# Optimization experiments

Hardware: AMD Instinct MI355X
Metric: run time of the kernel (lower is better)

The kernel has to match this reference:

```python
import jax, jax.numpy as jnp
import numpy as np

B, SL, H = 8, 512, 768
NS, W = 256, 32            # num_spans, max_span_width (static pad width)
NH = 12
HD = H // NH
FFN_I = int(H * 4)         # int(output_dim * ffn_ratio)
LN_EPS = 1e-5
NEG = -1e9


def _pos_encoding(seq_len, hidden):
    pos = jnp.arange(seq_len, dtype=jnp.float32)[:, None]
    div = jnp.exp(jnp.arange(0, hidden, 2, dtype=jnp.float32) * (-np.log(10000.0) / hidden))
    pe = jnp.zeros((seq_len, hidden), jnp.float32)
    pe = pe.at[:, 0::2].set(jnp.sin(pos * div))
    pe = pe.at[:, 1::2].set(jnp.cos(pos * div))
    return pe


def _layernorm(x, g, b):
    mu = jnp.mean(x, axis=-1, keepdims=True)
    var = jnp.mean(jnp.square(x - mu), axis=-1, keepdims=True)
    return (x - mu) * jax.lax.rsqrt(var + LN_EPS) * g + b


def setup_inputs() -> dict:
    key = jax.random.key(0)
    ks = jax.random.split(key, 16)
    token_reps = jax.random.normal(ks[0], (B, SL, H), jnp.float32)
    starts = jax.random.randint(ks[1], (B, NS), 0, SL - W)
    widths = jax.random.randint(ks[2], (B, NS), 0, W + 1)  # includes empty spans
    span_ids = jnp.stack([starts, starts + widths], axis=-1).astype(jnp.int64)
    s = 0.02
    return {
        "token_reps": token_reps,
        "span_ids": span_ids,
        "dummy_query": jax.random.normal(ks[3], (1, 1, H), jnp.float32),
        "in_proj_w": jax.random.normal(ks[4], (3 * H, H), jnp.float32) * s,
        "in_proj_b": jnp.zeros((3 * H,), jnp.float32),
        "out_proj_w": jax.random.normal(ks[5], (H, H), jnp.float32) * s,
        "out_proj_b": jnp.zeros((H,), jnp.float32),
        "ln_g": jnp.ones((H,), jnp.float32),
        "ln_b": jnp.zeros((H,), jnp.float32),
        "ffn_w1": jax.random.normal(ks[6], (FFN_I, H), jnp.float32) * s,
        "ffn_b1": jnp.zeros((FFN_I,), jnp.float32),
        "ffn_w2": jax.random.normal(ks[7], (H, FFN_I), jnp.float32) * s,
        "ffn_b2": jnp.zeros((H,), jnp.float32),
        "pooling": 1,
    }


def reference(token_reps, span_ids, dummy_query, in_proj_w, in_proj_b,
              out_proj_w, out_proj_b, ln_g, ln_b,
              ffn_w1, ffn_b1, ffn_w2, ffn_b2, pooling):
    # sequence positional encoding (dropout=0 / eval mode)
    pe = _pos_encoding(SL, H)
    tok = token_reps + pe[None, :, :]

    starts = span_ids[..., 0]                        # (B, NS)
    lengths = span_ids[..., 1] - span_ids[..., 0]    # (B, NS)
    offs = jnp.arange(W)
    pos = starts[..., None] + offs                   # (B, NS, W)
    valid = offs[None, None, :] < lengths[..., None] # (B, NS, W) bool
    idx = jnp.clip(pos, 0, SL - 1)
    # vectorized span gather -> padded tensor (B, NS, W, H), zeros on padding
    spans = tok[jnp.arange(B)[:, None, None], idx]
    spans = spans * valid[..., None].astype(tok.dtype)

    N = B * NS
    spans = spans.reshape(N, W, H)
    valid_f = valid.reshape(N, W)

    Wq, Wk, Wv = jnp.split(in_proj_w, 3, axis=0)
    bq, bk, bv = jnp.split(in_proj_b, 3, axis=0)

    q0 = dummy_query[0, 0]                            # (H,)
    q = (q0 @ Wq.T + bq).reshape(NH, HD)              # (NH, HD)
    k = (spans @ Wk.T + bk).reshape(N, W, NH, HD)
    v = (spans @ Wv.T + bv).reshape(N, W, NH, HD)

    scores = jnp.einsum('hd,nwhd->nhw', q, k) / np.sqrt(HD)
    scores = jnp.where(valid_f[:, None, :], scores, NEG)
    attn = jax.nn.softmax(scores, axis=-1)            # (N, NH, W)
    ctx = jnp.einsum('nhw,nwhd->nhd', attn, v).reshape(N, H)
    attn_out = ctx @ out_proj_w.T + out_proj_b        # (N, H)

    x = _layernorm(attn_out + q0, ln_g, ln_b)
    h = jnp.maximum(x @ ffn_w1.T + ffn_b1, 0.0)
    x = _layernorm((h @ ffn_w2.T + ffn_b2) + x, ln_g, ln_b)

    out = x.reshape(B, NS, H)
    out = jnp.where((lengths > 0)[..., None], out, 0.0)
    return out
```

## Files before the change

### kernel.cpp

```cpp
#include <hip/hip_runtime.h>
#include <hip/hip_bf16.h>
#include <cstdint>

#define Bb 8
#define SLh 512
#define Hh 768
#define NSs 256
#define Ww 32
#define NHh 12
#define HDd 64
#define FFN_I 3072
#define NTOK (Bb*SLh)
#define NSPAN (Bb*NSs)
#define NVS 832

typedef __attribute__((ext_vector_type(8))) __bf16 bf16x8;
typedef __attribute__((ext_vector_type(4))) float f32x4;

__device__ __forceinline__ short f2bf(float f) {
  unsigned u = __builtin_bit_cast(unsigned, f);
  unsigned r = (u + 0x7fffu + ((u >> 16) & 1u)) >> 16;
  return (short)r;
}
__device__ __forceinline__ float bflo(unsigned u) { return __builtin_bit_cast(float, u << 16); }
__device__ __forceinline__ float bfhi(unsigned u) { return __builtin_bit_cast(float, u & 0xffff0000u); }

__device__ __forceinline__ void gload16(const void* g, void* l) {
  __builtin_amdgcn_global_load_lds(
      (__attribute__((address_space(1))) void*)(const_cast<void*>(g)),
      (__attribute__((address_space(3))) void*)l, 16, 0, 0);
}

__global__ __launch_bounds__(192) void tok_kernel(const float* __restrict__ tr,
                                                  short* __restrict__ tok) {
  int row = blockIdx.x;
  int s = row & (SLh - 1);
  int c0 = threadIdx.x * 4;
  float4 v = *(const float4*)(tr + (size_t)row * Hh + c0);
  const float kinv = -9.210340371976184f / (float)Hh;
  float f0 = __expf((float)c0 * kinv);
  float f1 = __expf((float)(c0 + 2) * kinv);
  float s0, cc0, s1, cc1;
  __sincosf((float)s * f0, &s0, &cc0);
  __sincosf((float)s * f1, &s1, &cc1);
  v.x += s0; v.y += cc0; v.z += s1; v.w += cc1;
  short4 o{f2bf(v.x), f2bf(v.y), f2bf(v.z), f2bf(v.w)};
  *(short4*)(tok + (size_t)row * Hh + c0) = o;
}

__global__ __launch_bounds__(256) void cast4(const float* __restrict__ s0,
                                             const float* __restrict__ s1,
                                             const float* __restrict__ s2,
                                             const float* __restrict__ s3,
                                             short* __restrict__ d0,
                                             short* __restrict__ d1,
                                             short* __restrict__ d2,
                                             short* __restrict__ d3) {
  int b = blockIdx.x;
  if (b >= 5760) {
    int i = (b - 5760) * 256 + threadIdx.x;
    ((short4*)d0)[149760 + i] = short4{0, 0, 0, 0};
    return;
  }
  const float* s; short* d; int off;
  if (b < 576)       { s = s0; d = d0; off = b; }
  else if (b < 1152) { s = s1; d = d1; off = b - 576; }
  else if (b < 3456) { s = s2; d = d2; off = b - 1152; }
  else               { s = s3; d = d3; off = b - 3456; }
  int i = off * 256 + threadIdx.x;
  float4 v = ((const float4*)s)[i];
  short4 o{f2bf(v.x), f2bf(v.y), f2bf(v.z), f2bf(v.w)};
  ((short4*)d)[i] = o;
}

__global__ __launch_bounds__(64) void prep_qb(const float* __restrict__ dq,
                                              const float* __restrict__ ipw,
                                              const float* __restrict__ ipb,
                                              const float* __restrict__ opb,
                                              float* __restrict__ qsv,
                                              float* __restrict__ bias2,
                                              float* __restrict__ bvs) {
  int b = blockIdx.x, lane = threadIdx.x;
  if (b == 12) { if (lane < 52) bvs[780 + lane] = 0.f; return; }
  int h = b * 64 + lane;
  const float4* wr = (const float4*)(ipw + (size_t)h * Hh);
  const float4* qv = (const float4*)dq;
  float acc = 0.f;
  for (int j = 0; j < Hh / 4; ++j) {
    float4 w4 = wr[j], q4 = qv[j];
    acc += w4.x * q4.x + w4.y * q4.y + w4.z * q4.z + w4.w * q4.w;
  }
  acc += ipb[h];
  float qs = acc * 0.125f;
  qsv[h] = qs;
  bias2[h] = opb[h] + dq[h];
  bvs[h] = ipb[2 * Hh + h];
  float t = qs * ipb[Hh + h];
#pragma unroll
  for (int o = 32; o; o >>= 1) t += __shfl_xor(t, o);
  if (lane == 0) bvs[768 + b] = t;
}

__global__ __launch_bounds__(64) void qk_kernel(const float* __restrict__ ipw,
                                                const float* __restrict__ qsv,
                                                short* __restrict__ vsw) {
  int h = blockIdx.x, dc = blockIdx.y, lane = threadIdx.x;
  int d = dc * 64 + lane;
  const float* wk = ipw + (size_t)(Hh + h * 64) * Hh + d;
  const float* qh = qsv + h * 64;
  float a = 0.f;
#pragma unroll 8
  for (int e = 0; e < 64; ++e) a += qh[e] * wk[(size_t)e * Hh];
  vsw[(size_t)(768 + h) * Hh + d] = f2bf(a);
}

template <int EPI, int BN>
__global__ __launch_bounds__(256, BN == 64 ? 3 : 2)
void gemm_bt(const short* __restrict__ A,
             const short* __restrict__ Bt,
             const float* __restrict__ bias,
             float* __restrict__ Cf,
             short* __restrict__ Cb,
             int M, int N, int ldk, int Kc,
             int nx, int ypp) {
  constexpr int NI = BN / 32;
  __shared__ __align__(16) char Al[2][128 * 128];
  __shared__ __align__(16) char Bl[2][BN * 128];
  const int tid = threadIdx.x;
  const int lane = tid & 63, wave = tid >> 6;
  const int wm = wave >> 1, wn = wave & 1;
  const int bid = blockIdx.x, xcd = bid & 7, ii = bid >> 3;
  const int iy = ii / nx;
  const int by = xcd * ypp + iy, bx = ii - iy * nx;
  const int row0 = by * 128, col0 = bx * BN;
  const int kbase = blockIdx.y * Kc;
  const int l15 = lane & 15, hi = lane >> 4;
  f32x4 acc[4][NI] = {};
  const int nk = Kc >> 6;
  const int srow = tid >> 3, sslot = tid & 7;

  auto stage = [&](int kt, int bi) {
    const short* Agp = A + (size_t)row0 * ldk + kbase + kt * 64;
    const short* Bgp = Bt + (size_t)col0 * ldk + kbase + kt * 64;
#pragma unroll
    for (int j = 0; j < 4; ++j) {
      int row = j * 32 + srow;
      int col = (sslot ^ (row & 7)) << 3;
      gload16(Agp + (size_t)row * ldk + col,
              &Al[bi][0] + (size_t)(j * 256 + wave * 64) * 16);
    }
#pragma unroll
    for (int j = 0; j < NI; ++j) {
      int row = j * 32 + srow;
      int col = (sslot ^ (row & 7)) << 3;
      gload16(Bgp + (size_t)row * ldk + col,
              &Bl[bi][0] + (size_t)(j * 256 + wave * 64) * 16);
    }
  };

  stage(0, 0);
  for (int kt = 0; kt < nk; ++kt) {
    const int cur = kt & 1;
    if (kt + 1 < nk) {
      stage(kt + 1, cur ^ 1);
      if constexpr (BN == 64)
        asm volatile("s_waitcnt vmcnt(6)" ::: "memory");
      else
        asm volatile("s_waitcnt vmcnt(8)" ::: "memory");
    } else {
      asm volatile("s_waitcnt vmcnt(0)" ::: "memory");
    }
    __builtin_amdgcn_s_barrier();
    asm volatile("" ::: "memory");
    bf16x8 fa[2][4], fb[2][NI];
#pragma unroll
    for (int kk = 0; kk < 2; ++kk) {
#pragma unroll
      for (int i = 0; i < 4; ++i) {
        int Ra = wm * 64 + i * 16 + l15;
        fa[kk][i] = *(const bf16x8*)(&Al[cur][0] + (size_t)Ra * 128 +
                                     (((kk * 4 + hi) ^ (Ra & 7)) << 4));
      }
#pragma unroll
      for (int i = 0; i < NI; ++i) {
        int Rb = wn * (BN / 2) + i * 16 + l15;
        fb[kk][i] = *(const bf16x8*)(&Bl[cur][0] + (size_t)Rb * 128 +
                                     (((kk * 4 + hi) ^ (Rb & 7)) << 4));
      }
    }
#pragma unroll
    for (int kk = 0; kk < 2; ++kk)
#pragma unroll
      for (int mi = 0; mi < 4; ++mi)
#pragma unroll
        for (int ni = 0; ni < NI; ++ni)
          acc[mi][ni] = __builtin_amdgcn_mfma_f32_16x16x32_bf16(fa[kk][mi], fb[kk][ni], acc[mi][ni], 0, 0, 0);
    asm volatile("" ::: "memory");
    __builtin_amdgcn_s_barrier();
  }

  float* dst = (EPI == 3) ? (Cf + (size_t)blockIdx.y * M * N) : Cf;
#pragma unroll
  for (int mi = 0; mi < 4; ++mi) {
#pragma unroll
    for (int ni = 0; ni < NI; ++ni) {
      int colb = col0 + wn * (BN / 2) + ni * 16 + l15;
      float bv = (EPI == 3) ? 0.f : bias[colb];
#pragma unroll
      for (int r = 0; r < 4; ++r) {
        int rowb = row0 + wm * 64 + mi * 16 + hi * 4 + r;
        float v = acc[mi][ni][r] + bv;
        if (EPI == 1) {
          Cb[(size_t)rowb * N + colb] = f2bf(fmaxf(v, 0.f));
        } else if (EPI == 3) {
          dst[(size_t)rowb * N + colb] = v;
        } else {
          if (colb < 768) Cb[(size_t)rowb * 768 + colb] = f2bf(v);
          else if (colb < 780) Cf[(size_t)rowb * 12 + (colb - 768)] = v;
        }
      }
    }
  }
}

__global__ __launch_bounds__(384) void attn_kernel(const short* __restrict__ Vb,
                                                   const float* __restrict__ S,
                                                   const int* __restrict__ sid,
                                                   short* __restrict__ ctx) {
  int bid = blockIdx.x;
  int n = ((bid & 7) << 8) | (bid >> 3);
  int b = n >> 8;
  __shared__ int posV[Ww], tS[Ww];
  __shared__ float attnL[NHh][Ww];
  __shared__ int lenS;
  int tid = threadIdx.x;
  if (tid < Ww) {
    int st = sid[2 * n], en = sid[2 * n + 1];
    int p = st + tid;
    p = p < 0 ? 0 : (p > SLh - 1 ? SLh - 1 : p);
    int t = b * SLh + p;
    posV[tid] = t * Hh;
    tS[tid] = t * 12;
    if (tid == 0) lenS = en - st;
  }
  __syncthreads();
  int len = lenS;
  int h = tid >> 5, w = tid & 31;
  float score = (w < len) ? S[tS[w] + h] : -1e9f;
  float m = score;
#pragma unroll
  for (int o = 16; o; o >>= 1) m = fmaxf(m, __shfl_xor(m, o, 32));
  float e = __expf(score - m);
  float ssum = e;
#pragma unroll
  for (int o = 16; o; o >>= 1) ssum += __shfl_xor(ssum, o, 32);
  attnL[h][w] = e / ssum;
  __syncthreads();
  int hh = tid >> 5, dp = tid & 31;
  float a0 = 0.f, a1 = 0.f;
#pragma unroll
  for (int w2 = 0; w2 < Ww; ++w2) {
    float aw = attnL[hh][w2];
    unsigned u = *(const unsigned*)(Vb + posV[w2] + hh * HDd + 2 * dp);
    a0 += aw * bflo(u);
    a1 += aw * bfhi(u);
  }
  unsigned packed = (unsigned)(unsigned short)f2bf(a0) | ((unsigned)(unsigned short)f2bf(a1) << 16);
  ((unsigned*)ctx)[(size_t)n * (Hh / 2) + tid] = packed;
}

__global__ __launch_bounds__(256) void ln_kernel(const float* __restrict__ Y2,
                                                 const float* __restrict__ bias2,
                                                 const float* __restrict__ g,
                                                 const float* __restrict__ b,
                                                 float* __restrict__ xf,
                                                 short* __restrict__ xb) {
  const size_t SL = (size_t)NSPAN * Hh;
  int row = blockIdx.x;
  int tid = threadIdx.x;
  float v[3]; float s1 = 0.f, s2 = 0.f;
#pragma unroll
  for (int i = 0; i < 3; ++i) {
    int c = tid + 256 * i;
    size_t idx = (size_t)row * Hh + c;
    v[i] = Y2[idx] + Y2[idx + SL] + bias2[c];
    s1 += v[i]; s2 += v[i] * v[i];
  }
  __shared__ float r1[4], r2[4];
#pragma unroll
  for (int o = 32; o; o >>= 1) { s1 += __shfl_xor(s1, o); s2 += __shfl_xor(s2, o); }
  int lane = tid & 63, wv = tid >> 6;
  if (lane == 0) { r1[wv] = s1; r2[wv] = s2; }
  __syncthreads();
  s1 = r1[0] + r1[1] + r1[2] + r1[3];
  s2 = r2[0] + r2[1] + r2[2] + r2[3];
  float mu = s1 * (1.f / Hh);
  float var = s2 * (1.f / Hh) - mu * mu;
  float is = rsqrtf(var + 1e-5f);
#pragma unroll
  for (int i = 0; i < 3; ++i) {
    int c = tid + 256 * i;
    float o = (v[i] - mu) * is * g[c] + b[c];
    xf[(size_t)row * Hh + c] = o;
    xb[(size_t)row * Hh + c] = f2bf(o);
  }
}

__global__ __launch_bounds__(256) void ln_final(const float* __restrict__ Y4,
                                                const float* __restrict__ b2,
                                                const float* __restrict__ xf,
                                                const float* __restrict__ g,
                                                const float* __restrict__ b,
                                                const int* __restrict__ sid,
                                                float* __restrict__ out) {
  const size_t SL = (size_t)NSPAN * Hh;
  int row = blockIdx.x;
  int len = sid[2 * row + 1] - sid[2 * row];
  int tid = threadIdx.x;
  float v[3]; float s1 = 0.f, s2 = 0.f;
#pragma unroll
  for (int i = 0; i < 3; ++i) {
    int c = tid + 256 * i;
    size_t idx = (size_t)row * Hh + c;
    v[i] = Y4[idx] + Y4[idx + SL] + Y4[idx + 2 * SL] + Y4[idx + 3 * SL]
         + b2[c] + xf[idx];
    s1 += v[i]; s2 += v[i] * v[i];
  }
  __shared__ float r1[4], r2[4];
#pragma unroll
  for (int o = 32; o; o >>= 1) { s1 += __shfl_xor(s1, o); s2 += __shfl_xor(s2, o); }
  int lane = tid & 63, wv = tid >> 6;
  if (lane == 0) { r1[wv] = s1; r2[wv] = s2; }
  __syncthreads();
  s1 = r1[0] + r1[1] + r1[2] + r1[3];
  s2 = r2[0] + r2[1] + r2[2] + r2[3];
  float mu = s1 * (1.f / Hh);
  float var = s2 * (1.f / Hh) - mu * mu;
  float is = rsqrtf(var + 1e-5f);
  float keep = (len > 0) ? 1.f : 0.f;
#pragma unroll
  for (int i = 0; i < 3; ++i) {
    int c = tid + 256 * i;
    float o = ((v[i] - mu) * is * g[c] + b[c]) * keep;
    out[(size_t)row * Hh + c] = o;
  }
}

extern "C" void kernel_launch(void* const* d_in, const int* in_sizes, int n_in,
                              void* d_out, int out_size, void* d_ws, size_t ws_size,
                              hipStream_t stream) {
  const float* token_reps = (const float*)d_in[0];
  const int* span_ids = (const int*)d_in[1];
  const float* dq = (const float*)d_in[2];
  const float* ipw = (const float*)d_in[3];
  const float* ipb = (const float*)d_in[4];
  const float* opw = (const float*)d_in[5];
  const float* opb = (const float*)d_in[6];
  const float* lng = (const float*)d_in[7];
  const float* lnb = (const float*)d_in[8];
  const float* w1 = (const float*)d_in[9];
  const float* b1 = (const float*)d_in[10];
  const float* w2 = (const float*)d_in[11];
  const float* b2 = (const float*)d_in[12];
  float* out = (float*)d_out;

  char* p = (char*)d_ws;
  auto alloc = [&](size_t bytes) { void* r = p; p += (bytes + 255) & ~(size_t)255; return r; };
  short* tokb = (short*)alloc((size_t)NTOK * Hh * 2);
  short* vsw  = (short*)alloc((size_t)NVS * Hh * 2);
  short* outw = (short*)alloc((size_t)Hh * Hh * 2);
  short* w1b  = (short*)alloc((size_t)FFN_I * Hh * 2);
  short* w2b  = (short*)alloc((size_t)Hh * FFN_I * 2);
  float* qsv  = (float*)alloc(Hh * 4);
  float* bias2= (float*)alloc(Hh * 4);
  float* bvs  = (float*)alloc(NVS * 4);
  float* S    = (float*)alloc((size_t)NTOK * 12 * 4);
  short* Vb   = (short*)alloc((size_t)NTOK * Hh * 2);
  short* ctxb = (short*)alloc((size_t)NSPAN * Hh * 2);
  float* attnY= (float*)alloc((size_t)2 * NSPAN * Hh * 4);
  float* xf   = (float*)alloc((size_t)NSPAN * Hh * 4);
  short* xb   = (short*)alloc((size_t)NSPAN * Hh * 2);
  short* hb   = (short*)alloc((size_t)NSPAN * FFN_I * 2);
  float* y2   = (float*)alloc((size_t)4 * NSPAN * Hh * 4);

  tok_kernel<<<NTOK, 192, 0, stream>>>(token_reps, tokb);
  cast4<<<5799, 256, 0, stream>>>(ipw + (size_t)2 * Hh * Hh, opw, w1, w2,
                                  vsw, outw, w1b, w2b);
  prep_qb<<<13, 64, 0, stream>>>(dq, ipw, ipb, opb, qsv, bias2, bvs);
  qk_kernel<<<dim3(12, 12), 64, 0, stream>>>(ipw, qsv, vsw);
  gemm_bt<4, 64><<<dim3(416, 1), 256, 0, stream>>>(tokb, vsw, bvs, S, Vb,
                                                   NTOK, NVS, Hh, Hh, 13, 4);
  attn_kernel<<<NSPAN, 384, 0, stream>>>(Vb, S, span_ids, ctxb);
  gemm_bt<3, 64><<<dim3(192, 2), 256, 0, stream>>>(ctxb, outw, nullptr, attnY, nullptr,
                                                   NSPAN, Hh, Hh, Hh / 2, 12, 2);
  ln_kernel<<<NSPAN, 256, 0, stream>>>(attnY, bias2, lng, lnb, xf, xb);
  gemm_bt<1, 128><<<dim3(384, 1), 256, 0, stream>>>(xb, w1b, b1, nullptr, hb,
                                                    NSPAN, FFN_I, Hh, Hh, 24, 2);
  gemm_bt<3, 128><<<dim3(96, 4), 256, 0, stream>>>(hb, w2b, nullptr, y2, nullptr,
                                                   NSPAN, Hh, FFN_I, FFN_I / 4, 6, 2);
  ln_final<<<NSPAN, 256, 0, stream>>>(y2, b2, xf, lng, lnb, span_ids, out);
}
```

Before: 204.2 us.

## Merge prep kernels, add BM template, retile FFN GEMMs and split out-proj K further

```diff
diff --git a/kernel.cpp b/kernel.cpp
--- a/kernel.cpp
+++ b/kernel.cpp
@@ -31,91 +31,88 @@
       (__attribute__((address_space(3))) void*)l, 16, 0, 0);
 }
 
-__global__ __launch_bounds__(192) void tok_kernel(const float* __restrict__ tr,
-                                                  short* __restrict__ tok) {
-  int row = blockIdx.x;
-  int s = row & (SLh - 1);
-  int c0 = threadIdx.x * 4;
-  float4 v = *(const float4*)(tr + (size_t)row * Hh + c0);
-  const float kinv = -9.210340371976184f / (float)Hh;
-  float f0 = __expf((float)c0 * kinv);
-  float f1 = __expf((float)(c0 + 2) * kinv);
-  float s0, cc0, s1, cc1;
-  __sincosf((float)s * f0, &s0, &cc0);
-  __sincosf((float)s * f1, &s1, &cc1);
-  v.x += s0; v.y += cc0; v.z += s1; v.w += cc1;
-  short4 o{f2bf(v.x), f2bf(v.y), f2bf(v.z), f2bf(v.w)};
-  *(short4*)(tok + (size_t)row * Hh + c0) = o;
-}
-
-__global__ __launch_bounds__(256) void cast4(const float* __restrict__ s0,
-                                             const float* __restrict__ s1,
-                                             const float* __restrict__ s2,
-                                             const float* __restrict__ s3,
-                                             short* __restrict__ d0,
-                                             short* __restrict__ d1,
-                                             short* __restrict__ d2,
-                                             short* __restrict__ d3) {
-  int b = blockIdx.x;
-  if (b >= 5760) {
-    int i = (b - 5760) * 256 + threadIdx.x;
-    ((short4*)d0)[149760 + i] = short4{0, 0, 0, 0};
+__global__ __launch_bounds__(256) void prep_all(const float* __restrict__ tr,
+                                                const float* __restrict__ wv,
+                                                const float* __restrict__ wo,
+                                                const float* __restrict__ w1,
+                                                const float* __restrict__ w2,
+                                                short* __restrict__ tok,
+                                                short* __restrict__ vsw,
+                                                short* __restrict__ outw,
+                                                short* __restrict__ w1b,
+                                                short* __restrict__ w2b) {
+  int b = blockIdx.x, tid = threadIdx.x;
+  if (b < 3072) {
+    int i4 = b * 256 + tid;
+    int row = i4 / 192;
+    int c0 = (i4 - row * 192) * 4;
+    int s = row & (SLh - 1);
+    float4 v = ((const float4*)tr)[i4];
+    const float kinv = -9.210340371976184f / (float)Hh;
+    float f0 = __expf((float)c0 * kinv);
+    float f1 = __expf((float)(c0 + 2) * kinv);
+    float s0, cc0, s1, cc1;
+    __sincosf((float)s * f0, &s0, &cc0);
+    __sincosf((float)s * f1, &s1, &cc1);
+    v.x += s0; v.y += cc0; v.z += s1; v.w += cc1;
+    ((short4*)tok)[i4] = short4{f2bf(v.x), f2bf(v.y), f2bf(v.z), f2bf(v.w)};
     return;
   }
+  if (b >= 8832) {
+    int i = (b - 8832) * 256 + tid;
+    ((short4*)vsw)[149760 + i] = short4{0, 0, 0, 0};
+    return;
+  }
   const float* s; short* d; int off;
-  if (b < 576)       { s = s0; d = d0; off = b; }
-  else if (b < 1152) { s = s1; d = d1; off = b - 576; }
-  else if (b < 3456) { s = s2; d = d2; off = b - 1152; }
-  else               { s = s3; d = d3; off = b - 3456; }
-  int i = off * 256 + threadIdx.x;
+  if (b < 3648)      { s = wv; d = vsw;  off = b - 3072; }
+  else if (b < 4224) { s = wo; d = outw; off = b - 3648; }
+  else if (b < 6528) { s = w1; d = w1b;  off = b - 4224; }
+  else               { s = w2; d = w2b;  off = b - 6528; }
+  int i = off * 256 + tid;
   float4 v = ((const float4*)s)[i];
-  short4 o{f2bf(v.x), f2bf(v.y), f2bf(v.z), f2bf(v.w)};
-  ((short4*)d)[i] = o;
-}
-
-__global__ __launch_bounds__(64) void prep_qb(const float* __restrict__ dq,
-                                              const float* __restrict__ ipw,
-                                              const float* __restrict__ ipb,
-                                              const float* __restrict__ opb,
-                                              float* __restrict__ qsv,
-                                              float* __restrict__ bias2,
-                                              float* __restrict__ bvs) {
-  int b = blockIdx.x, lane = threadIdx.x;
-  if (b == 12) { if (lane < 52) bvs[780 + lane] = 0.f; return; }
-  int h = b * 64 + lane;
-  const float4* wr = (const float4*)(ipw + (size_t)h * Hh);
+  ((short4*)d)[i] = short4{f2bf(v.x), f2bf(v.y), f2bf(v.z), f2bf(v.w)};
+}
+
+__global__ __launch_bounds__(64) void qkprep(const float* __restrict__ dq,
+                                             const float* __restrict__ ipw,
+                                             const float* __restrict__ ipb,
+                                             const float* __restrict__ opb,
+                                             float* __restrict__ bias2,
+                                             float* __restrict__ bvs,
+                                             short* __restrict__ vsw) {
+  int h = blockIdx.x, dc = blockIdx.y, lane = threadIdx.x;
+  int hl = h * 64 + lane;
+  const float4* wr = (const float4*)(ipw + (size_t)hl * Hh);
   const float4* qv = (const float4*)dq;
   float acc = 0.f;
   for (int j = 0; j < Hh / 4; ++j) {
     float4 w4 = wr[j], q4 = qv[j];
     acc += w4.x * q4.x + w4.y * q4.y + w4.z * q4.z + w4.w * q4.w;
   }
-  acc += ipb[h];
-  float qs = acc * 0.125f;
-  qsv[h] = qs;
-  bias2[h] = opb[h] + dq[h];
-  bvs[h] = ipb[2 * Hh + h];
-  float t = qs * ipb[Hh + h];
-#pragma unroll
-  for (int o = 32; o; o >>= 1) t += __shfl_xor(t, o);
-  if (lane == 0) bvs[768 + b] = t;
-}
-
-__global__ __launch_bounds__(64) void qk_kernel(const float* __restrict__ ipw,
-                                                const float* __restrict__ qsv,
-                                                short* __restrict__ vsw) {
-  int h = blockIdx.x, dc = blockIdx.y, lane = threadIdx.x;
+  float qs = (acc + ipb[hl]) * 0.125f;
+  if (dc == 12) {
+    bias2[hl] = opb[hl] + dq[hl];
+    bvs[hl] = ipb[2 * Hh + hl];
+    float t = qs * ipb[Hh + hl];
+#pragma unroll
+    for (int o = 32; o; o >>= 1) t += __shfl_xor(t, o);
+    if (lane == 0) bvs[768 + h] = t;
+    if (h == 0 && lane < 52) bvs[780 + lane] = 0.f;
+    return;
+  }
+  __shared__ float qh[64];
+  qh[lane] = qs;
+  __syncthreads();
   int d = dc * 64 + lane;
   const float* wk = ipw + (size_t)(Hh + h * 64) * Hh + d;
-  const float* qh = qsv + h * 64;
   float a = 0.f;
 #pragma unroll 8
   for (int e = 0; e < 64; ++e) a += qh[e] * wk[(size_t)e * Hh];
   vsw[(size_t)(768 + h) * Hh + d] = f2bf(a);
 }
 
-template <int EPI, int BN>
-__global__ __launch_bounds__(256, BN == 64 ? 3 : 2)
+template <int EPI, int BM, int BN>
+__global__ __launch_bounds__(256, 3)
 void gemm_bt(const short* __restrict__ A,
              const short* __restrict__ Bt,
              const float* __restrict__ bias,
@@ -123,8 +120,8 @@
              short* __restrict__ Cb,
              int M, int N, int ldk, int Kc,
              int nx, int ypp) {
-  constexpr int NI = BN / 32;
-  __shared__ __align__(16) char Al[2][128 * 128];
+  constexpr int MI = BM / 32, NI = BN / 32;
+  __shared__ __align__(16) char Al[2][BM * 128];
   __shared__ __align__(16) char Bl[2][BN * 128];
   const int tid = threadIdx.x;
   const int lane = tid & 63, wave = tid >> 6;
@@ -132,10 +129,10 @@
   const int bid = blockIdx.x, xcd = bid & 7, ii = bid >> 3;
   const int iy = ii / nx;
   const int by = xcd * ypp + iy, bx = ii - iy * nx;
-  const int row0 = by * 128, col0 = bx * BN;
+  const int row0 = by * BM, col0 = bx * BN;
   const int kbase = blockIdx.y * Kc;
   const int l15 = lane & 15, hi = lane >> 4;
-  f32x4 acc[4][NI] = {};
+  f32x4 acc[MI][NI] = {};
   const int nk = Kc >> 6;
   const int srow = tid >> 3, sslot = tid & 7;
 
@@ -143,7 +140,7 @@
     const short* Agp = A + (size_t)row0 * ldk + kbase + kt * 64;
     const short* Bgp = Bt + (size_t)col0 * ldk + kbase + kt * 64;
 #pragma unroll
-    for (int j = 0; j < 4; ++j) {
+    for (int j = 0; j < MI; ++j) {
       int row = j * 32 + srow;
       int col = (sslot ^ (row & 7)) << 3;
       gload16(Agp + (size_t)row * ldk + col,
@@ -163,21 +160,18 @@
     const int cur = kt & 1;
     if (kt + 1 < nk) {
       stage(kt + 1, cur ^ 1);
-      if constexpr (BN == 64)
-        asm volatile("s_waitcnt vmcnt(6)" ::: "memory");
-      else
-        asm volatile("s_waitcnt vmcnt(8)" ::: "memory");
+      asm volatile("s_waitcnt vmcnt(6)" ::: "memory");
     } else {
       asm volatile("s_waitcnt vmcnt(0)" ::: "memory");
     }
     __builtin_amdgcn_s_barrier();
     asm volatile("" ::: "memory");
-    bf16x8 fa[2][4], fb[2][NI];
+    bf16x8 fa[2][MI], fb[2][NI];
 #pragma unroll
     for (int kk = 0; kk < 2; ++kk) {
 #pragma unroll
-      for (int i = 0; i < 4; ++i) {
-        int Ra = wm * 64 + i * 16 + l15;
+      for (int i = 0; i < MI; ++i) {
+        int Ra = wm * (BM / 2) + i * 16 + l15;
         fa[kk][i] = *(const bf16x8*)(&Al[cur][0] + (size_t)Ra * 128 +
                                      (((kk * 4 + hi) ^ (Ra & 7)) << 4));
       }
@@ -191,7 +185,7 @@
 #pragma unroll
     for (int kk = 0; kk < 2; ++kk)
 #pragma unroll
-      for (int mi = 0; mi < 4; ++mi)
+      for (int mi = 0; mi < MI; ++mi)
 #pragma unroll
         for (int ni = 0; ni < NI; ++ni)
           acc[mi][ni] = __builtin_amdgcn_mfma_f32_16x16x32_bf16(fa[kk][mi], fb[kk][ni], acc[mi][ni], 0, 0, 0);
@@ -201,14 +195,14 @@
 
   float* dst = (EPI == 3) ? (Cf + (size_t)blockIdx.y * M * N) : Cf;
 #pragma unroll
-  for (int mi = 0; mi < 4; ++mi) {
+  for (int mi = 0; mi < MI; ++mi) {
 #pragma unroll
     for (int ni = 0; ni < NI; ++ni) {
       int colb = col0 + wn * (BN / 2) + ni * 16 + l15;
       float bv = (EPI == 3) ? 0.f : bias[colb];
 #pragma unroll
       for (int r = 0; r < 4; ++r) {
-        int rowb = row0 + wm * 64 + mi * 16 + hi * 4 + r;
+        int rowb = row0 + wm * (BM / 2) + mi * 16 + hi * 4 + r;
         float v = acc[mi][ni][r] + bv;
         if (EPI == 1) {
           Cb[(size_t)rowb * N + colb] = f2bf(fmaxf(v, 0.f));
@@ -269,7 +263,7 @@
   ((unsigned*)ctx)[(size_t)n * (Hh / 2) + tid] = packed;
 }
 
-__global__ __launch_bounds__(256) void ln_kernel(const float* __restrict__ Y2,
+__global__ __launch_bounds__(256) void ln_kernel(const float* __restrict__ Y4,
                                                  const float* __restrict__ bias2,
                                                  const float* __restrict__ g,
                                                  const float* __restrict__ b,
@@ -283,7 +277,7 @@
   for (int i = 0; i < 3; ++i) {
     int c = tid + 256 * i;
     size_t idx = (size_t)row * Hh + c;
-    v[i] = Y2[idx] + Y2[idx + SL] + bias2[c];
+    v[i] = Y4[idx] + Y4[idx + SL] + Y4[idx + 2 * SL] + Y4[idx + 3 * SL] + bias2[c];
     s1 += v[i]; s2 += v[i] * v[i];
   }
   __shared__ float r1[4], r2[4];
@@ -371,32 +365,29 @@
   short* outw = (short*)alloc((size_t)Hh * Hh * 2);
   short* w1b  = (short*)alloc((size_t)FFN_I * Hh * 2);
   short* w2b  = (short*)alloc((size_t)Hh * FFN_I * 2);
-  float* qsv  = (float*)alloc(Hh * 4);
   float* bias2= (float*)alloc(Hh * 4);
   float* bvs  = (float*)alloc(NVS * 4);
   float* S    = (float*)alloc((size_t)NTOK * 12 * 4);
   short* Vb   = (short*)alloc((size_t)NTOK * Hh * 2);
   short* ctxb = (short*)alloc((size_t)NSPAN * Hh * 2);
-  float* attnY= (float*)alloc((size_t)2 * NSPAN * Hh * 4);
+  float* attnY= (float*)alloc((size_t)4 * NSPAN * Hh * 4);
   float* xf   = (float*)alloc((size_t)NSPAN * Hh * 4);
   short* xb   = (short*)alloc((size_t)NSPAN * Hh * 2);
   short* hb   = (short*)alloc((size_t)NSPAN * FFN_I * 2);
   float* y2   = (float*)alloc((size_t)4 * NSPAN * Hh * 4);
 
-  tok_kernel<<<NTOK, 192, 0, stream>>>(token_reps, tokb);
-  cast4<<<5799, 256, 0, stream>>>(ipw + (size_t)2 * Hh * Hh, opw, w1, w2,
-                                  vsw, outw, w1b, w2b);
-  prep_qb<<<13, 64, 0, stream>>>(dq, ipw, ipb, opb, qsv, bias2, bvs);
-  qk_kernel<<<dim3(12, 12), 64, 0, stream>>>(ipw, qsv, vsw);
-  gemm_bt<4, 64><<<dim3(416, 1), 256, 0, stream>>>(tokb, vsw, bvs, S, Vb,
-                                                   NTOK, NVS, Hh, Hh, 13, 4);
+  prep_all<<<8871, 256, 0, stream>>>(token_reps, ipw + (size_t)2 * Hh * Hh, opw,
+                                     w1, w2, tokb, vsw, outw, w1b, w2b);
+  qkprep<<<dim3(12, 13), 64, 0, stream>>>(dq, ipw, ipb, opb, bias2, bvs, vsw);
+  gemm_bt<4, 128, 64><<<dim3(416, 1), 256, 0, stream>>>(tokb, vsw, bvs, S, Vb,
+                                                        NTOK, NVS, Hh, Hh, 13, 4);
   attn_kernel<<<NSPAN, 384, 0, stream>>>(Vb, S, span_ids, ctxb);
-  gemm_bt<3, 64><<<dim3(192, 2), 256, 0, stream>>>(ctxb, outw, nullptr, attnY, nullptr,
-                                                   NSPAN, Hh, Hh, Hh / 2, 12, 2);
+  gemm_bt<3, 128, 64><<<dim3(192, 4), 256, 0, stream>>>(ctxb, outw, nullptr, attnY, nullptr,
+                                                        NSPAN, Hh, Hh, Hh / 4, 12, 2);
   ln_kernel<<<NSPAN, 256, 0, stream>>>(attnY, bias2, lng, lnb, xf, xb);
-  gemm_bt<1, 128><<<dim3(384, 1), 256, 0, stream>>>(xb, w1b, b1, nullptr, hb,
-                                                    NSPAN, FFN_I, Hh, Hh, 24, 2);
-  gemm_bt<3, 128><<<dim3(96, 4), 256, 0, stream>>>(hb, w2b, nullptr, y2, nullptr,
-                                                   NSPAN, Hh, FFN_I, FFN_I / 4, 6, 2);
+  gemm_bt<1, 64, 128><<<dim3(768, 1), 256, 0, stream>>>(xb, w1b, b1, nullptr, hb,
+                                                        NSPAN, FFN_I, Hh, Hh, 24, 4);
+  gemm_bt<3, 64, 128><<<dim3(192, 4), 256, 0, stream>>>(hb, w2b, nullptr, y2, nullptr,
+                                                        NSPAN, Hh, FFN_I, FFN_I / 4, 6, 4);
   ln_final<<<NSPAN, 256, 0, stream>>>(y2, b2, xf, lng, lnb, span_ids, out);
 }
```

Result: no change. 200.3 us (-1.9%).
